# Optimization experiments

Measured on AMD Instinct MI355X. Metric: run time of the kernel, lower is better.

## Reference

```python
import jax, jax.numpy as jnp
import numpy as np
from math import factorial

N_ATOM = 32768
NODE_DIM = 128
HID = 64
MUL = 16          # hidden multiplicity per irrep
INS = [(0,0,0),(0,2,2),(1,1,0),(1,1,1),(1,1,2),(2,0,2),(2,2,0),(2,2,1),(2,2,2)]  # (l1,l2,l_out)
W_NUMEL = len(INS)*MUL*MUL  # 2304 per-sample tp weights

# ---------- real Clebsch-Gordan coefficients (e3nn-style, Frobenius-normalized) ----------
def _su2_cg(j1,j2,j3,m1,m2,m3):
    if m3 != m1+m2 or not (abs(j1-j2) <= j3 <= j1+j2):
        return 0.0
    f = factorial
    pref = np.sqrt((2*j3+1)*f(j3+j1-j2)*f(j3-j1+j2)*f(j1+j2-j3)/f(j1+j2+j3+1))
    pref *= np.sqrt(f(j3+m3)*f(j3-m3)*f(j1-m1)*f(j1+m1)*f(j2-m2)*f(j2+m2))
    s = 0.0
    for v in range(max(0, j2-j3-m1, j1-j3+m2), min(j1+j2-j3, j1-m1, j2+m2)+1):
        s += (-1)**v/(f(v)*f(j1+j2-j3-v)*f(j1-m1-v)*f(j2+m2-v)*f(j3-j2+m1+v)*f(j3-j1-m2+v))
    return pref*s

def _r2c(l):
    q = np.zeros((2*l+1,2*l+1), dtype=complex)
    for m in range(-l, 0):
        q[l+m, l+abs(m)] = 1/np.sqrt(2); q[l+m, l-abs(m)] = -1j/np.sqrt(2)
    q[l, l] = 1.0
    for m in range(1, l+1):
        q[l+m, l+abs(m)] = (-1)**m/np.sqrt(2); q[l+m, l-abs(m)] = 1j*(-1)**m/np.sqrt(2)
    return (-1j)**l * q

def real_cg(l1, l2, l3):
    C = np.zeros((2*l1+1,2*l2+1,2*l3+1), dtype=complex)
    for m1 in range(-l1, l1+1):
        for m2 in range(-l2, l2+1):
            m3 = m1+m2
            if abs(m3) <= l3:
                C[l1+m1, l2+m2, l3+m3] = _su2_cg(l1,l2,l3,m1,m2,m3)
    Cr = np.einsum('ij,kl,nm,ikn->jlm', _r2c(l1), _r2c(l2), np.conj(_r2c(l3)), C)
    re, im = np.real(Cr), np.imag(Cr)
    out = re if np.linalg.norm(re) >= np.linalg.norm(im) else im
    return (out / np.linalg.norm(out)).astype(np.float32)

_CG = {ins: real_cg(*ins) for ins in set(INS)}
# change of basis: irreps 1x0e+1x1e+1x2e (dim 9) -> cartesian 3x3 rank-2 tensor
_QF = np.concatenate([np.sqrt(2*l+1)*real_cg(l,1,1) for l in range(3)], 0).reshape(9,9).astype(np.float32)
_PERM = np.array([2,0,1])  # e3nn (y,z,x) -> cartesian (x,y,z)


def setup_inputs() -> dict:
    key = jax.random.key(0)
    ks = jax.random.split(key, 12)
    n = lambda k, s: jax.random.normal(k, s, dtype=jnp.float32)
    return {
        "x_scalar": n(ks[0], (N_ATOM, NODE_DIM)),
        "x_spherical": n(ks[1], (N_ATOM, 128 + 64*3 + 32*5)),
        "w_pre0": n(ks[2], (128, MUL)),
        "w_pre1": n(ks[3], (64, MUL)),
        "w_pre2": n(ks[4], (32, MUL)),
        "gw1": n(ks[5], (NODE_DIM, HID)) / float(np.sqrt(NODE_DIM)),
        "gb1": jnp.zeros((HID,), jnp.float32),
        "gw2": n(ks[6], (HID, W_NUMEL)) / float(np.sqrt(HID)),
        "gb2": jnp.zeros((W_NUMEL,), jnp.float32),
        "wpost0": n(ks[7], (3*MUL, 1)),
        "wpost1": n(ks[8], (2*MUL, 1)),
        "wpost2": n(ks[9], (4*MUL, 1)),
    }


def reference(x_scalar, x_spherical, w_pre0, w_pre1, w_pre2, gw1, gb1, gw2, gb2, wpost0, wpost1, wpost2):
    N = x_scalar.shape[0]
    # split edge irreps 128x0e + 64x1o + 32x2e
    x0 = x_spherical[:, :128]
    x1 = x_spherical[:, 128:320].reshape(N, 64, 3)
    x2 = x_spherical[:, 320:].reshape(N, 32, 5)
    # pre o3.Linear (per-l channel mixing, fan-in normalized)
    h = [
        (x0 @ w_pre0)[:, :, None] / float(np.sqrt(128.0)),              # [N,16,1] 0e
        jnp.einsum('num,uv->nvm', x1, w_pre1) / float(np.sqrt(64.0)),    # [N,16,3] 1o
        jnp.einsum('num,uv->nvm', x2, w_pre2) / float(np.sqrt(32.0)),    # [N,16,5] 2e
    ]
    # gate MLP -> per-sample tp weights [N, n_ins, u, w]
    g = (jax.nn.silu(x_scalar @ gw1 + gb1) @ gw2 + gb2).reshape(N, len(INS), MUL, MUL)
    # 'uuw' CG tensor product
    outs = {0: [], 1: [], 2: []}
    inv_sqrt_mul = float(1.0 / np.sqrt(MUL))
    for idx, (i, j, lo) in enumerate(INS):
        C = jnp.asarray(_CG[(i, j, lo)])
        o = jnp.einsum('nuw,abm,nua,nub->nwm', g[:, idx], C, h[i], h[j]) * inv_sqrt_mul
        outs[lo].append(o)
    # post o3.Linear: (48x0e + 32x1e + 64x2e) -> 1x0e + 1x1e + 1x2e
    wpost = [wpost0, wpost1, wpost2]
    ys = []
    for lo in range(3):
        z = jnp.concatenate(outs[lo], axis=1)                       # [N, n_paths*MUL, 2lo+1]
        y = jnp.einsum('num,uv->nvm', z, wpost[lo]) / float(np.sqrt(z.shape[1]))
        ys.append(y.reshape(N, 2*lo+1))
    atom_out = jnp.concatenate(ys, axis=1)                           # [N,9]
    # change of basis to cartesian rank-2 tensor + axis reindexing
    res = (atom_out @ jnp.asarray(_QF)).reshape(N, 3, 3)
    return res[:, _PERM][:, :, _PERM]
```

## Files before the change

### kernel.cpp

```cpp
#include <hip/hip_runtime.h>

#define NA 32768

typedef float  f32x4  __attribute__((ext_vector_type(4)));
typedef __bf16 bf16x8 __attribute__((ext_vector_type(8)));
typedef unsigned short u16x8 __attribute__((ext_vector_type(8)));


__device__ __forceinline__ unsigned short bf16u(float f) {
    unsigned int x = __float_as_uint(f);
    x += 0x7FFFu + ((x >> 16) & 1u);
    return (unsigned short)(x >> 16);
}
__device__ __forceinline__ unsigned short cvt1(float f) {
    return __builtin_bit_cast(unsigned short, (__bf16)f);
}
__device__ __forceinline__ f32x4 MFMA16(u16x8 a, u16x8 b, f32x4 c) {
    return __builtin_amdgcn_mfma_f32_16x16x32_bf16(
        __builtin_bit_cast(bf16x8, a), __builtin_bit_cast(bf16x8, b), c, 0, 0, 0);
}

__global__ void setup_kernel(const float* __restrict__ gw1,
                             const float* __restrict__ gw2, const float* __restrict__ gb2,
                             const float* __restrict__ w_pre0, const float* __restrict__ w_pre1,
                             const float* __restrict__ w_pre2,
                             const float* __restrict__ wpost0, const float* __restrict__ wpost1,
                             const float* __restrict__ wpost2,
                             unsigned short* __restrict__ wsS, float* __restrict__ b2p)
{
    const int t = blockIdx.x * 256 + threadIdx.x;
    const int LO[9]  = {0,2,0,1,2,2,0,1,2};
    const int POS[9] = {0,0,1,0,1,2,2,1,3};
    const float SCALE[3] = {0.036084391824351615f,
                            0.04419417382415922f,
                            0.03125f};
    if (t < 8192) {
        const int j = t & 7, lane = (t >> 3) & 63, kt = (t >> 9) & 3, ct = t >> 11;
        const int k = kt * 32 + ((lane >> 4) & 3) * 8 + j;
        const int n = ct * 16 + (lane & 15);
        wsS[t] = bf16u(gw1[k * 64 + n]);
    } else if (t < 17408) {
        const int q = t - 8192;
        const int j = q & 7, lane = (q >> 3) & 63, kt = (q >> 9) & 1, ct = q >> 10;
        const int k = kt * 32 + ((lane >> 4) & 3) * 8 + j;
        const int idx = ct, u = lane & 15;
        const int lo = LO[idx];
        const float* wp = (lo == 0) ? wpost0 : (lo == 1) ? wpost1 : wpost2;
        const float* wv = wp + POS[idx] * 16;
        const float* gsrc = gw2 + (size_t)k * 2304 + idx * 256 + u * 16;
        float s = 0.f;
        for (int w = 0; w < 16; ++w) s = fmaf(gsrc[w], wv[w], s);
        wsS[8192 + q] = bf16u(s * SCALE[lo]);
    } else if (t < 19456) {
        const int q = t - 17408;
        const int j = q & 7, lane = (q >> 3) & 63, kt = q >> 9;
        const int k = kt * 32 + ((lane >> 4) & 3) * 8 + j;
        wsS[17408 + q] = bf16u(w_pre0[k * 16 + (lane & 15)] * 0.08838834764831845f);
    } else if (t < 20480) {
        const int q = t - 19456;
        const int j = q & 7, lane = (q >> 3) & 63, kt = q >> 9;
        const int k = kt * 32 + ((lane >> 4) & 3) * 8 + j;
        wsS[19456 + q] = bf16u(w_pre1[k * 16 + (lane & 15)] * 0.125f);
    } else if (t < 20992) {
        const int q = t - 20480;
        const int j = q & 7, lane = (q >> 3) & 63;
        const int k = ((lane >> 4) & 3) * 8 + j;
        wsS[20480 + q] = bf16u(w_pre2[k * 16 + (lane & 15)] * 0.17677669529663687f);
    } else if (t < 21136) {
        const int e = t - 20992;
        const int idx = e >> 4, u = e & 15;
        const int lo = LO[idx];
        const float* wp = (lo == 0) ? wpost0 : (lo == 1) ? wpost1 : wpost2;
        const float* wv = wp + POS[idx] * 16;
        const float* bsrc = gb2 + idx * 256 + u * 16;
        float sb = 0.f;
        for (int w = 0; w < 16; ++w) sb = fmaf(bsrc[w], wv[w], sb);
        b2p[e] = sb * SCALE[lo];
    }
}

__global__ __launch_bounds__(256) void csc_kernel(
    const float* __restrict__ x_scalar, const float* __restrict__ x_sph,
    const float* __restrict__ gb1,
    const unsigned short* __restrict__ wsS, const float* __restrict__ b2p,
    float* __restrict__ out)
{
    __shared__ __align__(16) unsigned short sH[4][16][72];

    const int lane = threadIdx.x & 63;
    const int wvi  = threadIdx.x >> 6;
    const int lm = lane & 15, lg = lane >> 4;
    const int n0 = (blockIdx.x * 4 + wvi) * 16;

    const float* __restrict__ rowq = x_sph + (size_t)(n0 + lm) * 480;

    float S0[32], S1[48], S2[40];
#pragma unroll
    for (int kt = 0; kt < 4; ++kt) {
        *(float4*)&S0[kt * 8]     = *(const float4*)(rowq + kt * 32 + lg * 8);
        *(float4*)&S0[kt * 8 + 4] = *(const float4*)(rowq + kt * 32 + lg * 8 + 4);
    }
#pragma unroll
    for (int kt = 0; kt < 2; ++kt)
#pragma unroll
        for (int c = 0; c < 6; ++c)
            *(float4*)&S1[kt * 24 + c * 4] =
                *(const float4*)(rowq + 128 + 96 * kt + 24 * lg + c * 4);
#pragma unroll
    for (int c = 0; c < 10; ++c)
        *(float4*)&S2[c * 4] = *(const float4*)(rowq + 320 + 40 * lg + c * 4);

    u16x8 f0[4];
#pragma unroll
    for (int kt = 0; kt < 4; ++kt)
#pragma unroll
        for (int j = 0; j < 8; ++j) f0[kt][j] = cvt1(S0[kt * 8 + j]);
    u16x8 f1[3][2];
#pragma unroll
    for (int m = 0; m < 3; ++m)
#pragma unroll
        for (int kt = 0; kt < 2; ++kt)
#pragma unroll
            for (int j = 0; j < 8; ++j) f1[m][kt][j] = cvt1(S1[kt * 24 + 3 * j + m]);
    u16x8 f2[5];
#pragma unroll
    for (int m = 0; m < 5; ++m)
#pragma unroll
        for (int j = 0; j < 8; ++j) f2[m][j] = cvt1(S2[5 * j + m]);

    f32x4 accA0, accA1, accA2, accA3;
    {
        const float b0 = gb1[lm], b1 = gb1[16 + lm], bv2 = gb1[32 + lm], b3 = gb1[48 + lm];
        accA0 = (f32x4){b0,b0,b0,b0}; accA1 = (f32x4){b1,b1,b1,b1};
        accA2 = (f32x4){bv2,bv2,bv2,bv2}; accA3 = (f32x4){b3,b3,b3,b3};
    }
#pragma unroll
    for (int kt = 0; kt < 4; ++kt) {
        const float* xr = x_scalar + (size_t)(n0 + lm) * 128 + kt * 32 + lg * 8;
        const float4 xa = *(const float4*)xr;
        const float4 xb = *(const float4*)(xr + 4);
        const u16x8 af = { cvt1(xa.x), cvt1(xa.y), cvt1(xa.z), cvt1(xa.w),
                           cvt1(xb.x), cvt1(xb.y), cvt1(xb.z), cvt1(xb.w) };
        accA0 = MFMA16(af, *(const u16x8*)(wsS + (size_t)((0*4+kt)*64+lane)*8), accA0);
        accA1 = MFMA16(af, *(const u16x8*)(wsS + (size_t)((1*4+kt)*64+lane)*8), accA1);
        accA2 = MFMA16(af, *(const u16x8*)(wsS + (size_t)((2*4+kt)*64+lane)*8), accA2);
        accA3 = MFMA16(af, *(const u16x8*)(wsS + (size_t)((3*4+kt)*64+lane)*8), accA3);
    }
#pragma unroll
    for (int r = 0; r < 4; ++r) {
        const int atom = lg * 4 + r;
        const float v0 = accA0[r], v1 = accA1[r], v2 = accA2[r], v3 = accA3[r];
        sH[wvi][atom][ 0 + lm] = cvt1(v0 / (1.f + __expf(-v0)));
        sH[wvi][atom][16 + lm] = cvt1(v1 / (1.f + __expf(-v1)));
        sH[wvi][atom][32 + lm] = cvt1(v2 / (1.f + __expf(-v2)));
        sH[wvi][atom][48 + lm] = cvt1(v3 / (1.f + __expf(-v3)));
    }

    const u16x8 hf0 = *(const u16x8*)&sH[wvi][lm][lg * 8];
    const u16x8 hf1 = *(const u16x8*)&sH[wvi][lm][32 + lg * 8];
    f32x4 gB0, gB1, gB2, gB4, gB5, gB6, gB8;
#define INITB(ACC, CT) { const float b = b2p[(CT)*16 + lm]; ACC = (f32x4){b,b,b,b}; }
    INITB(gB0,0) INITB(gB1,1) INITB(gB2,2) INITB(gB4,4) INITB(gB5,5) INITB(gB6,6) INITB(gB8,8)
#define DOB(ACC, CT) \
    ACC = MFMA16(hf0, *(const u16x8*)(wsS + 8192 + (size_t)(((CT)*2+0)*64+lane)*8), ACC); \
    ACC = MFMA16(hf1, *(const u16x8*)(wsS + 8192 + (size_t)(((CT)*2+1)*64+lane)*8), ACC);
    DOB(gB0,0) DOB(gB1,1) DOB(gB2,2) DOB(gB4,4) DOB(gB5,5) DOB(gB6,6) DOB(gB8,8)

    f32x4 acc0 = (f32x4){0.f,0.f,0.f,0.f};
#pragma unroll
    for (int kt = 0; kt < 4; ++kt)
        acc0 = MFMA16(f0[kt], *(const u16x8*)(wsS + 17408 + (size_t)(kt*64+lane)*8), acc0);
    f32x4 accP[3];
#pragma unroll
    for (int m = 0; m < 3; ++m) {
        f32x4 acc = (f32x4){0.f,0.f,0.f,0.f};
#pragma unroll
        for (int kt = 0; kt < 2; ++kt)
            acc = MFMA16(f1[m][kt], *(const u16x8*)(wsS + 19456 + (size_t)(kt*64+lane)*8), acc);
        accP[m] = acc;
    }
    f32x4 accQ[5];
#pragma unroll
    for (int m = 0; m < 5; ++m)
        accQ[m] = MFMA16(f2[m], *(const u16x8*)(wsS + 20480 + (size_t)lane*8),
                         (f32x4){0.f,0.f,0.f,0.f});

    const float C110 = 0.5773502691896258f;
    const float C220 = 0.4472135954999579f;
    const float Ca = 0.31622776601683794f, Cb = 0.18257418583505536f;
    const float A2 = 0.2390457218668787f, B2c = 0.20701966780270626f, D2 = 0.11952286093343936f;
    const float is3 = 0.5773502691896258f, is6 = 0.4082482904638631f, is2 = 0.7071067811865476f;

#pragma unroll
    for (int r = 0; r < 4; ++r) {
        const int row = lg * 4 + r;
        const float h0 = acc0[r];
        const float p0 = accP[0][r], p1 = accP[1][r], p2 = accP[2][r];
        const float q0 = accQ[0][r], q1 = accQ[1][r], q2 = accQ[2][r],
                    q3 = accQ[3][r], q4 = accQ[4][r];
        const float G0 = gB0[r], G1 = gB1[r], G2 = gB2[r], G4 = gB4[r],
                    G5 = gB5[r], G6 = gB6[r], G8 = gB8[r];

        float y0 = G0 * h0 * h0
                 + G2 * C110 * (p0*p0 + p1*p1 + p2*p2)
                 + G6 * C220 * (q0*q0 + q1*q1 + q2*q2 + q3*q3 + q4*q4);
        float z0, z1, z2, z3, z4;
        {
            const float c15 = C220 * h0 * (G1 + G5);
            z0 = c15 * q0; z1 = c15 * q1; z2 = c15 * q2; z3 = c15 * q3; z4 = c15 * q4;
        }
        z0 = fmaf(G4, 2.f*Ca*p0*p2, z0);
        z1 = fmaf(G4, 2.f*Ca*p0*p1, z1);
        z2 = fmaf(G4, Cb*(2.f*p1*p1 - p0*p0 - p2*p2), z2);
        z3 = fmaf(G4, 2.f*Ca*p2*p1, z3);
        z4 = fmaf(G4, Ca*(p2*p2 - p0*p0), z4);
        z0 = fmaf(G8, -2.f*A2*q0*q2 + 2.f*B2c*q1*q3, z0);
        z1 = fmaf(G8,  2.f*B2c*(q0*q3 - q4*q1) + 2.f*D2*q1*q2, z1);
        z2 = fmaf(G8,  A2*(q2*q2 - q0*q0 - q4*q4) + D2*(q1*q1 + q3*q3), z2);
        z3 = fmaf(G8,  2.f*B2c*(q0*q1 + q3*q4) + 2.f*D2*q2*q3, z3);
        z4 = fmaf(G8, -2.f*A2*q2*q4 + B2c*(q3*q3 - q1*q1), z4);

#pragma unroll
        for (int msk = 1; msk <= 8; msk <<= 1) {
            y0 += __shfl_xor(y0, msk, 64);
            z0 += __shfl_xor(z0, msk, 64);
            z1 += __shfl_xor(z1, msk, 64);
            z2 += __shfl_xor(z2, msk, 64);
            z3 += __shfl_xor(z3, msk, 64);
            z4 += __shfl_xor(z4, msk, 64);
        }

        const float c0 = y0*is3 - z2*is6 - z4*is2;
        const float c4 = y0*is3 + 2.f*z2*is6;
        const float c8 = y0*is3 - z2*is6 + z4*is2;
        const float c1 = z1*is2, c2v = z0*is2, c5 = z3*is2;
        if (lm < 9) {
            const float val = (lm==0)?c8 : (lm==1)?c2v : (lm==2)?c5 : (lm==3)?c2v
                            : (lm==4)?c0 : (lm==5)?c1 : (lm==6)?c5 : (lm==7)?c1 : c4;
            out[(size_t)(n0 + row) * 9 + lm] = val;
        }
    }
}

extern "C" void kernel_launch(void* const* d_in, const int* in_sizes, int n_in,
                              void* d_out, int out_size, void* d_ws, size_t ws_size,
                              hipStream_t stream) {
    const float* x_scalar = (const float*)d_in[0];
    const float* x_sph    = (const float*)d_in[1];
    const float* w_pre0   = (const float*)d_in[2];
    const float* w_pre1   = (const float*)d_in[3];
    const float* w_pre2   = (const float*)d_in[4];
    const float* gw1      = (const float*)d_in[5];
    const float* gb1      = (const float*)d_in[6];
    const float* gw2      = (const float*)d_in[7];
    const float* gb2      = (const float*)d_in[8];
    const float* wpost0   = (const float*)d_in[9];
    const float* wpost1   = (const float*)d_in[10];
    const float* wpost2   = (const float*)d_in[11];

    unsigned short* wsS = (unsigned short*)d_ws;
    float* b2p = (float*)((char*)d_ws + 41984);

    setup_kernel<<<83, 256, 0, stream>>>(gw1, gw2, gb2, w_pre0, w_pre1, w_pre2,
                                         wpost0, wpost1, wpost2, wsS, b2p);
    csc_kernel<<<NA / 64, 256, 0, stream>>>(x_scalar, x_sph, gb1, wsS, b2p, (float*)d_out);
}
```

Baseline: 29.33 us.

## Stage input rows through LDS with coalesced loads and bf16 conversion

Replaces the per-lane strided row reads of x_spherical and x_scalar with fully coalesced wave-wide float4 loads. Each value is converted to bf16 once and written into a per-wave LDS buffer, and the MFMA fragments (including the de-interleaved m components) are read back from LDS. The pre-linear MFMAs are also moved ahead of the scalar gate MLP so the same LDS buffer can be reused. The cost is a larger shared-memory footprint (about 70KB per block), which may lower occupancy, plus extra LDS traffic and possible bank conflicts from the odd row strides.

```diff
diff --git a/kernel.cpp b/kernel.cpp
--- a/kernel.cpp
+++ b/kernel.cpp
@@ -5,6 +5,7 @@
 typedef float  f32x4  __attribute__((ext_vector_type(4)));
 typedef __bf16 bf16x8 __attribute__((ext_vector_type(8)));
 typedef unsigned short u16x8 __attribute__((ext_vector_type(8)));
+typedef unsigned short u16x4 __attribute__((ext_vector_type(4)));
 
 
 __device__ __forceinline__ unsigned short bf16u(float f) {
@@ -79,54 +80,107 @@
     }
 }
 
+#define ROWQ 488
+#define ROWS 136
+#define SHOFF 7808
+
 __global__ __launch_bounds__(256) void csc_kernel(
     const float* __restrict__ x_scalar, const float* __restrict__ x_sph,
     const float* __restrict__ gb1,
     const unsigned short* __restrict__ wsS, const float* __restrict__ b2p,
     float* __restrict__ out)
 {
-    __shared__ __align__(16) unsigned short sH[4][16][72];
+    __shared__ __align__(16) unsigned short buf[4][8960];
 
     const int lane = threadIdx.x & 63;
     const int wvi  = threadIdx.x >> 6;
     const int lm = lane & 15, lg = lane >> 4;
     const int n0 = (blockIdx.x * 4 + wvi) * 16;
-
-    const float* __restrict__ rowq = x_sph + (size_t)(n0 + lm) * 480;
-
-    float S0[32], S1[48], S2[40];
-#pragma unroll
-    for (int kt = 0; kt < 4; ++kt) {
-        *(float4*)&S0[kt * 8]     = *(const float4*)(rowq + kt * 32 + lg * 8);
-        *(float4*)&S0[kt * 8 + 4] = *(const float4*)(rowq + kt * 32 + lg * 8 + 4);
-    }
-#pragma unroll
-    for (int kt = 0; kt < 2; ++kt)
-#pragma unroll
-        for (int c = 0; c < 6; ++c)
-            *(float4*)&S1[kt * 24 + c * 4] =
-                *(const float4*)(rowq + 128 + 96 * kt + 24 * lg + c * 4);
-#pragma unroll
-    for (int c = 0; c < 10; ++c)
-        *(float4*)&S2[c * 4] = *(const float4*)(rowq + 320 + 40 * lg + c * 4);
+    unsigned short* __restrict__ B = buf[wvi];
+
+    {
+        const float* __restrict__ src = x_sph + (size_t)n0 * 480;
+#pragma unroll
+        for (int i = 0; i < 30; ++i) {
+            const int idx4 = i * 64 + lane;
+            const int row = idx4 / 120, col4 = idx4 - row * 120;
+            const float4 v = *(const float4*)(src + (size_t)idx4 * 4);
+            const u16x4 w = { cvt1(v.x), cvt1(v.y), cvt1(v.z), cvt1(v.w) };
+            *(u16x4*)&B[row * ROWQ + col4 * 4] = w;
+        }
+    }
 
     u16x8 f0[4];
 #pragma unroll
     for (int kt = 0; kt < 4; ++kt)
-#pragma unroll
-        for (int j = 0; j < 8; ++j) f0[kt][j] = cvt1(S0[kt * 8 + j]);
+        f0[kt] = *(const u16x8*)&B[lm * ROWQ + kt * 32 + lg * 8];
     u16x8 f1[3][2];
 #pragma unroll
-    for (int m = 0; m < 3; ++m)
+    for (int kt = 0; kt < 2; ++kt) {
+        const int base = lm * ROWQ + 128 + 96 * kt + 24 * lg;
+        const u16x8 sA = *(const u16x8*)&B[base];
+        const u16x8 sB = *(const u16x8*)&B[base + 8];
+        const u16x8 sC = *(const u16x8*)&B[base + 16];
+        unsigned short span[24];
+#pragma unroll
+        for (int e = 0; e < 8; ++e) { span[e] = sA[e]; span[8 + e] = sB[e]; span[16 + e] = sC[e]; }
+#pragma unroll
+        for (int m = 0; m < 3; ++m) {
+            u16x8 f;
+#pragma unroll
+            for (int j = 0; j < 8; ++j) f[j] = span[3 * j + m];
+            f1[m][kt] = f;
+        }
+    }
+    u16x8 f2[5];
+    {
+        const int base = lm * ROWQ + 320 + 40 * lg;
+        unsigned short span[40];
+#pragma unroll
+        for (int c = 0; c < 5; ++c) {
+            const u16x8 s = *(const u16x8*)&B[base + c * 8];
+#pragma unroll
+            for (int e = 0; e < 8; ++e) span[c * 8 + e] = s[e];
+        }
+#pragma unroll
+        for (int m = 0; m < 5; ++m) {
+            u16x8 f;
+#pragma unroll
+            for (int j = 0; j < 8; ++j) f[j] = span[5 * j + m];
+            f2[m] = f;
+        }
+    }
+
+    f32x4 acc0 = (f32x4){0.f,0.f,0.f,0.f};
+#pragma unroll
+    for (int kt = 0; kt < 4; ++kt)
+        acc0 = MFMA16(f0[kt], *(const u16x8*)(wsS + 17408 + (size_t)(kt*64+lane)*8), acc0);
+    f32x4 accP[3];
+#pragma unroll
+    for (int m = 0; m < 3; ++m) {
+        f32x4 acc = (f32x4){0.f,0.f,0.f,0.f};
 #pragma unroll
         for (int kt = 0; kt < 2; ++kt)
-#pragma unroll
-            for (int j = 0; j < 8; ++j) f1[m][kt][j] = cvt1(S1[kt * 24 + 3 * j + m]);
-    u16x8 f2[5];
+            acc = MFMA16(f1[m][kt], *(const u16x8*)(wsS + 19456 + (size_t)(kt*64+lane)*8), acc);
+        accP[m] = acc;
+    }
+    f32x4 accQ[5];
 #pragma unroll
     for (int m = 0; m < 5; ++m)
-#pragma unroll
-        for (int j = 0; j < 8; ++j) f2[m][j] = cvt1(S2[5 * j + m]);
+        accQ[m] = MFMA16(f2[m], *(const u16x8*)(wsS + 20480 + (size_t)lane*8),
+                         (f32x4){0.f,0.f,0.f,0.f});
+
+    {
+        const float* __restrict__ src = x_scalar + (size_t)n0 * 128;
+#pragma unroll
+        for (int i = 0; i < 8; ++i) {
+            const int idx4 = i * 64 + lane;
+            const int row = idx4 >> 5, col4 = idx4 & 31;
+            const float4 v = *(const float4*)(src + (size_t)idx4 * 4);
+            const u16x4 w = { cvt1(v.x), cvt1(v.y), cvt1(v.z), cvt1(v.w) };
+            *(u16x4*)&B[row * ROWS + col4 * 4] = w;
+        }
+    }
 
     f32x4 accA0, accA1, accA2, accA3;
     {
@@ -136,11 +190,7 @@
     }
 #pragma unroll
     for (int kt = 0; kt < 4; ++kt) {
-        const float* xr = x_scalar + (size_t)(n0 + lm) * 128 + kt * 32 + lg * 8;
-        const float4 xa = *(const float4*)xr;
-        const float4 xb = *(const float4*)(xr + 4);
-        const u16x8 af = { cvt1(xa.x), cvt1(xa.y), cvt1(xa.z), cvt1(xa.w),
-                           cvt1(xb.x), cvt1(xb.y), cvt1(xb.z), cvt1(xb.w) };
+        const u16x8 af = *(const u16x8*)&B[lm * ROWS + kt * 32 + lg * 8];
         accA0 = MFMA16(af, *(const u16x8*)(wsS + (size_t)((0*4+kt)*64+lane)*8), accA0);
         accA1 = MFMA16(af, *(const u16x8*)(wsS + (size_t)((1*4+kt)*64+lane)*8), accA1);
         accA2 = MFMA16(af, *(const u16x8*)(wsS + (size_t)((2*4+kt)*64+lane)*8), accA2);
@@ -150,14 +200,14 @@
     for (int r = 0; r < 4; ++r) {
         const int atom = lg * 4 + r;
         const float v0 = accA0[r], v1 = accA1[r], v2 = accA2[r], v3 = accA3[r];
-        sH[wvi][atom][ 0 + lm] = cvt1(v0 / (1.f + __expf(-v0)));
-        sH[wvi][atom][16 + lm] = cvt1(v1 / (1.f + __expf(-v1)));
-        sH[wvi][atom][32 + lm] = cvt1(v2 / (1.f + __expf(-v2)));
-        sH[wvi][atom][48 + lm] = cvt1(v3 / (1.f + __expf(-v3)));
-    }
-
-    const u16x8 hf0 = *(const u16x8*)&sH[wvi][lm][lg * 8];
-    const u16x8 hf1 = *(const u16x8*)&sH[wvi][lm][32 + lg * 8];
+        B[SHOFF + atom * 72 +  0 + lm] = cvt1(v0 / (1.f + __expf(-v0)));
+        B[SHOFF + atom * 72 + 16 + lm] = cvt1(v1 / (1.f + __expf(-v1)));
+        B[SHOFF + atom * 72 + 32 + lm] = cvt1(v2 / (1.f + __expf(-v2)));
+        B[SHOFF + atom * 72 + 48 + lm] = cvt1(v3 / (1.f + __expf(-v3)));
+    }
+
+    const u16x8 hf0 = *(const u16x8*)&B[SHOFF + lm * 72 + lg * 8];
+    const u16x8 hf1 = *(const u16x8*)&B[SHOFF + lm * 72 + 32 + lg * 8];
     f32x4 gB0, gB1, gB2, gB4, gB5, gB6, gB8;
 #define INITB(ACC, CT) { const float b = b2p[(CT)*16 + lm]; ACC = (f32x4){b,b,b,b}; }
     INITB(gB0,0) INITB(gB1,1) INITB(gB2,2) INITB(gB4,4) INITB(gB5,5) INITB(gB6,6) INITB(gB8,8)
@@ -165,25 +215,6 @@
     ACC = MFMA16(hf0, *(const u16x8*)(wsS + 8192 + (size_t)(((CT)*2+0)*64+lane)*8), ACC); \
     ACC = MFMA16(hf1, *(const u16x8*)(wsS + 8192 + (size_t)(((CT)*2+1)*64+lane)*8), ACC);
     DOB(gB0,0) DOB(gB1,1) DOB(gB2,2) DOB(gB4,4) DOB(gB5,5) DOB(gB6,6) DOB(gB8,8)
-
-    f32x4 acc0 = (f32x4){0.f,0.f,0.f,0.f};
-#pragma unroll
-    for (int kt = 0; kt < 4; ++kt)
-        acc0 = MFMA16(f0[kt], *(const u16x8*)(wsS + 17408 + (size_t)(kt*64+lane)*8), acc0);
-    f32x4 accP[3];
-#pragma unroll
-    for (int m = 0; m < 3; ++m) {
-        f32x4 acc = (f32x4){0.f,0.f,0.f,0.f};
-#pragma unroll
-        for (int kt = 0; kt < 2; ++kt)
-            acc = MFMA16(f1[m][kt], *(const u16x8*)(wsS + 19456 + (size_t)(kt*64+lane)*8), acc);
-        accP[m] = acc;
-    }
-    f32x4 accQ[5];
-#pragma unroll
-    for (int m = 0; m < 5; ++m)
-        accQ[m] = MFMA16(f2[m], *(const u16x8*)(wsS + 20480 + (size_t)lane*8),
-                         (f32x4){0.f,0.f,0.f,0.f});
 
     const float C110 = 0.5773502691896258f;
     const float C220 = 0.4472135954999579f;
```

Result: faster. 27.56 us (-6.0%).
